# Kernel tuning notes

Measured on AMD Instinct MI355X. Metric: run time of the kernel, lower is better.

The kernel has to match this reference:

```python
import jax, jax.numpy as jnp
import numpy as np

H = 256
LATENT = 128
NODE_FEATS = (12, 5, 4)
EDGE_FEATS = (5, 4)
END_NODE = NODE_FEATS[0] - 1
MAX_NODES = 64


def setup_inputs() -> dict:
    key = jax.random.key(0)
    ks = iter(jax.random.split(key, 40))
    def rn(shape, s=0.1):
        return jax.random.normal(next(ks), shape, dtype=jnp.float32) * s
    inp = {
        "z": jax.random.normal(next(ks), (1, LATENT), dtype=jnp.float32),
        "lp_w": rn((H, LATENT)), "lp_b": rn((H,)),
        "nWih": rn((3 * H, H)), "nWhh": rn((3 * H, H)), "nbih": rn((3 * H,)), "nbhh": rn((3 * H,)),
        "eWih": rn((3 * H, H)), "eWhh": rn((3 * H, H)), "ebih": rn((3 * H,)), "ebhh": rn((3 * H,)),
    }
    for j, f in enumerate(NODE_FEATS):
        inp[f"nc{j}_w"] = rn((f, H)); inp[f"nc{j}_b"] = rn((f,))
    for j, f in enumerate(EDGE_FEATS):
        inp[f"ec{j}_w"] = rn((f, H)); inp[f"ec{j}_b"] = rn((f,))
    inp["max_nodes"] = MAX_NODES
    return inp


def _gru(x, h, Wih, Whh, bih, bhh):
    # torch.nn.GRU single step, single layer. x,h: (1,H)
    gi = x @ Wih.T + bih
    gh = h @ Whh.T + bhh
    ir, iz, inn = jnp.split(gi, 3, axis=-1)
    hr, hz, hn = jnp.split(gh, 3, axis=-1)
    r = jax.nn.sigmoid(ir + hr)
    zg = jax.nn.sigmoid(iz + hz)
    n = jnp.tanh(inn + r * hn)
    return (1.0 - zg) * n + zg * h


def _classify(emb, W, b):
    # Linear -> softmax -> (max prob, argmax), batch=1 -> scalars
    p = jax.nn.softmax(emb @ W.T + b, axis=-1)[0]
    return jnp.max(p), jnp.argmax(p)


def _generate(z, lp_w, lp_b, nWih, nWhh, nbih, nbhh, eWih, eWhh, ebih, ebhh,
              nc0_w, nc0_b, nc1_w, nc1_b, nc2_w, nc2_b,
              ec0_w, ec0_b, ec1_w, ec1_b, max_nodes):
    node_cls = ((nc0_w, nc0_b), (nc1_w, nc1_b), (nc2_w, nc2_b))
    edge_cls = ((ec0_w, ec0_b), (ec1_w, ec1_b))
    h0 = z @ lp_w.T + lp_b                     # latent_project; set_context
    buf0 = jnp.zeros((max_nodes, 1, H), z.dtype)  # node embedding history

    def step(carry, i):
        h, buf, done = carry
        x = jnp.where(i == 0, jnp.zeros((1, H), z.dtype), buf[jnp.maximum(i - 1, 0)])
        h1 = _gru(x, h, nWih, nWhh, nbih, nbhh)   # node_celli.forward_unit; emb = h1
        nps, nis = zip(*[_classify(h1, W, b) for W, b in node_cls])
        nprobs = jnp.stack(nps)                   # (3,)
        nidxs = jnp.stack(nis)                    # (3,) int
        is_end = nidxs[0] == END_NODE

        # edge cell: seq over previous node embeddings, most recent first
        def estep(he, t):
            valid = t < i
            src = jnp.clip(i - 1 - t, 0, max_nodes - 1)
            he2 = _gru(buf[src], he, eWih, eWhh, ebih, ebhh)
            he_new = jnp.where(valid, he2, he)
            eps, eis = zip(*[_classify(he_new, W, b) for W, b in edge_cls])
            return he_new, (jnp.stack(eps), jnp.stack(eis))

        he_fin, (ep_t, ei_t) = jax.lax.scan(estep, h1, jnp.arange(max_nodes))
        # reindex: edge for source node j was produced at inner step t = i-1-j
        js = jnp.arange(max_nodes)
        ts = jnp.clip(i - 1 - js, 0, max_nodes - 1)
        ep_row = ep_t[ts]                          # (max_nodes, 2)
        ei_row = ei_t[ts]
        vj = js < i
        no_edges = jnp.all(jnp.where(vj, ei_row[:, 0] == 0, True)) & (i > 0)

        active = jnp.logical_not(done)
        node_ok = active & jnp.logical_not(is_end) & jnp.logical_not(no_edges)
        done_new = done | is_end | no_edges

        h_next = jnp.where(node_ok & (i > 0), he_fin, h1)  # node hidden <- edge hidden
        h_next = jnp.where(active, h_next, h)
        buf_new = buf.at[i].set(jnp.where(node_ok, h1, buf[i]))

        edge_valid = vj & node_ok & (i > 0)
        out = (jnp.where(node_ok, nprobs, 0.0), nidxs, node_ok,
               jnp.where(edge_valid[:, None], ep_row, 0.0), ei_row, edge_valid)
        return (h_next, buf_new, done_new), out

    _, outs = jax.lax.scan(step, (h0, buf0, jnp.zeros((), bool)), jnp.arange(max_nodes))
    # node_probs (M,3), node_idxs (M,3), node_valid (M,),
    # edge_probs (M,M,2), edge_idxs (M,M,2), edge_valid (M,M)
    return outs


def reference(z, lp_w, lp_b, nWih, nWhh, nbih, nbhh, eWih, eWhh, ebih, ebhh,
              nc0_w, nc0_b, nc1_w, nc1_b, nc2_w, nc2_b,
              ec0_w, ec0_b, ec1_w, ec1_b, max_nodes):
    return _generate(z, lp_w, lp_b, nWih, nWhh, nbih, nbhh, eWih, eWhh, ebih, ebhh,
                     nc0_w, nc0_b, nc1_w, nc1_b, nc2_w, nc2_b,
                     ec0_w, ec0_b, ec1_w, ec1_b, max_nodes)
```

## Files before the change

kernel.cpp:

```cpp
#include <hip/hip_runtime.h>
#include <stdint.h>
#include <cstddef>


typedef unsigned int u32;

#define H 256
#define HL 128
#define G3 768
#define NW 16
#define SL 16
#define MAXN 64
#define NSTATE (1 + MAXN + (MAXN*(MAXN-1))/2)
#define SENTU 0xFFFFFFFFu
#define DEADV 0x0000DEADu

#define WG_CLS NW
#define WG_HELP0 (NW+1)
#define NHELP_PER 6
#define NROLE (WG_HELP0 + 2*NHELP_PER)
#define NWG 256

#define NP_OFF 0
#define NI_OFF 192
#define NV_OFF 384
#define EP_OFF 448
#define EI_OFF (EP_OFF + MAXN*MAXN*2)
#define EV_OFF (EI_OFF + MAXN*MAXN*2)

struct Wksp {
  float hP[NSTATE][H];
  float hS[NSTATE][H];
  float gi_e[MAXN][G3];
  float gi_n[MAXN][G3];
  u32 decP[MAXN];
  u32 decS[MAXN];
  u32 winner;
  u32 padw[7];
  u32 ticket[8];
};

union Shm {
  float force[26624];
  struct {
    float hcur[2][H];
    float bihe[3*SL], bhhe[3*SL], bihn[3*SL], bhhn[3*SL];
    float zv[HL];
    u32 dec;
  } w;
  struct {
    float cb[30];
    float hc[2][H];
    float logits[32];
    float np[3]; int ni[3];
    float ept[MAXN][2];
    int   eit[MAXN][2];
    u32 isend, bflag;
  } c;
  struct { float h1[H]; } hp;
};

__device__ __forceinline__ u32 ld_sc0(const u32* p) {
  u32 v;
  asm volatile("global_load_dword %0, %1, off sc0\n\ts_waitcnt vmcnt(0)"
               : "=&v"(v) : "v"(p) : "memory");
  return v;
}
__device__ __forceinline__ void st_sc0(u32* p, u32 v) {
  asm volatile("global_store_dword %0, %1, off sc0" :: "v"(p), "v"(v) : "memory");
}
__device__ __forceinline__ u32 ld_ag(const u32* p) {
  return __hip_atomic_load(p, __ATOMIC_RELAXED, __HIP_MEMORY_SCOPE_AGENT);
}
__device__ __forceinline__ void st_ag(u32* p, u32 v) {
  __hip_atomic_store(p, v, __ATOMIC_RELAXED, __HIP_MEMORY_SCOPE_AGENT);
}
__device__ __forceinline__ void pub2(u32* pp, u32* sp, u32 v, bool sc) {
  if (sc) st_sc0(pp, v);
  st_ag(sp, v);
}
__device__ __forceinline__ u32 spin2(const u32* pp, const u32* sp, bool sc) {
  if (sc) {
    #pragma unroll 1
    for (int i = 0; i < 16; ++i) {
      const u32 v = ld_sc0(pp);
      if (v != SENTU) return v;
    }
  }
  u32 v = ld_ag(sp);
  while (v == SENTU) v = ld_ag(sp);
  return v;
}
__device__ __forceinline__ float spin2f(const float* pp, const float* sp, bool sc) {
  return __uint_as_float(spin2((const u32*)pp, (const u32*)sp, sc));
}
__device__ __forceinline__ float spinf(const float* p) {
  u32 v = ld_ag((const u32*)p);
  while (v == SENTU) v = ld_ag((const u32*)p);
  return __uint_as_float(v);
}
__device__ __forceinline__ float spinf_slow(const float* p) {
  u32 v = ld_ag((const u32*)p);
  while (v == SENTU) {
    __builtin_amdgcn_s_sleep(1);
    v = ld_ag((const u32*)p);
  }
  return __uint_as_float(v);
}
__device__ __forceinline__ void pubf(float* p, float x) { st_ag((u32*)p, __float_as_uint(x)); }
__device__ __forceinline__ float sigm(float x) { return 1.0f / (1.0f + expf(-x)); }

__global__ __launch_bounds__(256, 1)
void Generator_34746285425383_kernel(
    const float* __restrict__ z, const float* __restrict__ lp_w, const float* __restrict__ lp_b,
    const float* __restrict__ nWih, const float* __restrict__ nWhh,
    const float* __restrict__ nbih, const float* __restrict__ nbhh,
    const float* __restrict__ eWih, const float* __restrict__ eWhh,
    const float* __restrict__ ebih, const float* __restrict__ ebhh,
    const float* __restrict__ nc0w, const float* __restrict__ nc0b,
    const float* __restrict__ nc1w, const float* __restrict__ nc1b,
    const float* __restrict__ nc2w, const float* __restrict__ nc2b,
    const float* __restrict__ ec0w, const float* __restrict__ ec0b,
    const float* __restrict__ ec1w, const float* __restrict__ ec1b,
    float* __restrict__ out, Wksp* __restrict__ ws)
{
  __shared__ Shm S;
  __shared__ int role_s, mode_s;
  const int tid = threadIdx.x;

  if (tid == 0) {
    u32 xcc;
    asm volatile("s_getreg_b32 %0, hwreg(HW_REG_XCC_ID)" : "=s"(xcc));
    xcc &= 7u;
    const u32 slot = __hip_atomic_fetch_add(&ws->ticket[xcc], 1u,
                        __ATOMIC_RELAXED, __HIP_MEMORY_SCOPE_AGENT);
    if (slot == NROLE - 1) {
      u32 exp = SENTU;
      __hip_atomic_compare_exchange_strong(&ws->winner, &exp, xcc,
          __ATOMIC_RELAXED, __ATOMIC_RELAXED, __HIP_MEMORY_SCOPE_AGENT);
    }
    u32 wv = ld_ag(&ws->winner);
    int iters = 0;
    while (wv == SENTU) {
      ++iters;
      if (iters > 1500 && blockIdx.x == 0) {
        u32 exp = SENTU;
        __hip_atomic_compare_exchange_strong(&ws->winner, &exp, DEADV,
            __ATOMIC_RELAXED, __ATOMIC_RELAXED, __HIP_MEMORY_SCOPE_AGENT);
      }
      wv = ld_ag(&ws->winner);
    }
    if (wv <= 7u) { role_s = (wv == xcc && slot < NROLE) ? (int)slot : -1; mode_s = 1; }
    else          { role_s = ((int)blockIdx.x < NROLE) ? (int)blockIdx.x : -1; mode_s = 0; }
  }
  __syncthreads();
  const int bid = role_s;
  const bool sc = (mode_s != 0);
  if (bid < 0) return;

  if (bid < NW) {
    const int w = bid, g = tid >> 4, c = tid & 15;
    const int k = w * SL + g;
    const bool gl = (c < 2);
    float wn0[16], wn1[16], wn2[16], we0[16], we1[16], we2[16];
    #pragma unroll
    for (int it = 0; it < 16; ++it) {
      const int col = c + 16 * it;
      wn0[it] = nWhh[(0 * H + k) * H + col];
      wn1[it] = nWhh[(1 * H + k) * H + col];
      wn2[it] = nWhh[(2 * H + k) * H + col];
      we0[it] = eWhh[(0 * H + k) * H + col];
      we1[it] = eWhh[(1 * H + k) * H + col];
      we2[it] = eWhh[(2 * H + k) * H + col];
    }
    if (tid < 3 * SL) {
      const int gate = tid / SL, gg = tid % SL;
      const int grow = gate * H + w * SL + gg;
      S.w.bihe[tid] = ebih[grow]; S.w.bhhe[tid] = ebhh[grow];
      S.w.bihn[tid] = nbih[grow]; S.w.bhhn[tid] = nbhh[grow];
    }
    if (tid < HL) S.w.zv[tid] = z[tid];
    __syncthreads();

    {
      float p = 0.f;
      for (int it = 0; it < 8; ++it) {
        const int col = c + 16 * it;
        p += S.w.zv[col] * lp_w[k * HL + col];
      }
      for (int off = 1; off < 16; off <<= 1) p += __shfl_xor(p, off);
      const float h0 = p + lp_b[k];
      if (c == 0 && sc) st_sc0((u32*)&ws->hP[0][k], __float_as_uint(h0));
      if (c == 1)       st_ag((u32*)&ws->hS[0][k], __float_as_uint(h0));
    }

    int m = 1, idx_carry = 0;
    bool done = false;
    unsigned long long valid = 0ull;
    float pg0 = 0.f, pg1 = 0.f, pg2 = 0.f;
    const float* pga = nullptr;

    for (int i = 0; i < MAXN; ++i) {
      for (int t = -1; t < i; ++t) {
        const bool is_node = (t < 0);
        const int hidx = is_node ? idx_carry : (m - 1);
        const int src  = is_node ? (i - 1) : (i - 1 - t);
        float* hc = S.w.hcur[m & 1];
        hc[tid] = spin2f(&ws->hP[hidx][tid], &ws->hS[hidx][tid], sc);
        float gi0 = 0.f, gi1 = 0.f, gi2 = 0.f;
        const bool use_gi = (src >= 0) && ((valid >> src) & 1ull);
        if (gl && use_gi) {
          gi0 = pg0; gi1 = pg1; gi2 = pg2;
          if (__float_as_uint(gi0) == SENTU) gi0 = spinf(&pga[0 * H + k]);
          if (__float_as_uint(gi1) == SENTU) gi1 = spinf(&pga[1 * H + k]);
          if (__float_as_uint(gi2) == SENTU) gi2 = spinf(&pga[2 * H + k]);
        }
        __syncthreads();
        float p0 = 0.f, p1 = 0.f, p2 = 0.f;
        if (is_node) {
          #pragma unroll
          for (int it = 0; it < 16; ++it) {
            const float hv = hc[c + 16 * it];
            p0 += wn0[it] * hv; p1 += wn1[it] * hv; p2 += wn2[it] * hv;
          }
        } else {
          #pragma unroll
          for (int it = 0; it < 16; ++it) {
            const float hv = hc[c + 16 * it];
            p0 += we0[it] * hv; p1 += we1[it] * hv; p2 += we2[it] * hv;
          }
        }
        for (int off = 1; off < 16; off <<= 1) {
          p0 += __shfl_xor(p0, off);
          p1 += __shfl_xor(p1, off);
          p2 += __shfl_xor(p2, off);
        }
        const float* bih = is_node ? S.w.bihn : S.w.bihe;
        const float* bhh = is_node ? S.w.bhhn : S.w.bhhe;
        const float rr = sigm(gi0 + bih[0 * SL + g] + p0 + bhh[0 * SL + g]);
        const float zz = sigm(gi1 + bih[1 * SL + g] + p1 + bhh[1 * SL + g]);
        const float nn = tanhf(gi2 + bih[2 * SL + g] + rr * (p2 + bhh[2 * SL + g]));
        const float hp = (1.f - zz) * nn + zz * hc[k];
        if (c == 0 && sc) st_sc0((u32*)&ws->hP[m][k], __float_as_uint(hp));
        if (c == 1)       st_ag((u32*)&ws->hS[m][k], __float_as_uint(hp));
        if (gl) {
          int ni = i, nt = t + 1;
          if (nt >= i) { ni = i + 1; nt = -1; }
          if (ni < MAXN) {
            const bool nnode = (nt < 0);
            const int nsrc = nnode ? (ni - 1) : (ni - 1 - nt);
            if (nsrc >= 0) {
              pga = nnode ? ws->gi_n[nsrc] : ws->gi_e[nsrc];
              pg0 = __builtin_nontemporal_load(&pga[0 * H + k]);
              pg1 = __builtin_nontemporal_load(&pga[1 * H + k]);
              pg2 = __builtin_nontemporal_load(&pga[2 * H + k]);
            }
          }
        }
        ++m;
      }
      if (tid == 0) S.w.dec = spin2(&ws->decP[i], &ws->decS[i], sc);
      __syncthreads();
      const u32 dec = S.w.dec;
      const bool is_end   = (dec >> 1) & 1u;
      const bool no_edges = (dec >> 2) & 1u;
      const bool active   = !done;
      const bool node_ok  = active && !is_end && !no_edges;
      if (node_ok) valid |= (1ull << i);
      const int s_end = m - 1, node_m = m - 1 - i;
      if (active) idx_carry = (node_ok && i > 0) ? s_end : node_m;
      done = done || is_end || no_edges;
    }

  } else if (bid == WG_CLS) {
    const int g = tid >> 4, c = tid & 15;
    const float* wsrc[5] = { nc0w, nc1w, nc2w, ec0w, ec1w };
    const float* bsrc[5] = { nc0b, nc1b, nc2b, ec0b, ec1b };
    const int hbase[5] = { 0, 12, 17, 21, 26 };
    float cw0[16], cw1[16];
    {
      const int r0 = g;
      const int h0i = r0 < 12 ? 0 : r0 < 17 ? 1 : r0 < 21 ? 2 : r0 < 26 ? 3 : 4;
      const float* W0 = wsrc[h0i];
      const int rr0 = r0 - hbase[h0i];
      const int r1 = g + 16;
      const int h1i = r1 < 17 ? 1 : r1 < 21 ? 2 : r1 < 26 ? 3 : 4;
      const float* W1 = wsrc[h1i];
      const int rr1 = r1 - hbase[h1i];
      const bool live1 = (r1 < 30);
      #pragma unroll
      for (int it = 0; it < 16; ++it) {
        const int col = c + 16 * it;
        cw0[it] = W0[rr0 * H + col];
        cw1[it] = live1 ? W1[rr1 * H + col] : 0.f;
      }
    }
    if (tid < 30) {
      const int hh = tid < 12 ? 0 : tid < 17 ? 1 : tid < 21 ? 2 : tid < 26 ? 3 : 4;
      S.c.cb[tid] = bsrc[hh][tid - hbase[hh]];
    }
    __syncthreads();

    int m = 1;
    bool done = false;
    for (int i = 0; i < MAXN; ++i) {
      for (int t = -1; t < i; ++t) {
        float* hcb = S.c.hc[m & 1];
        hcb[tid] = spin2f(&ws->hP[m][tid], &ws->hS[m][tid], sc);
        __syncthreads();
        {
          float p0 = 0.f, p1 = 0.f;
          #pragma unroll
          for (int it = 0; it < 16; ++it) {
            const float hv = hcb[c + 16 * it];
            p0 += cw0[it] * hv;
            p1 += cw1[it] * hv;
          }
          for (int off = 1; off < 16; off <<= 1) {
            p0 += __shfl_xor(p0, off);
            p1 += __shfl_xor(p1, off);
          }
          if (c == 0) {
            S.c.logits[g] = p0 + S.c.cb[g];
            if (g + 16 < 30) S.c.logits[g + 16] = p1 + S.c.cb[g + 16];
          }
        }
        __syncthreads();
        if (tid < 64) {
          const int lane = tid;
          int hh, j;
          if (lane < 16)      { hh = 0; j = lane;      }
          else if (lane < 24) { hh = 1; j = lane - 16; }
          else if (lane < 32) { hh = 2; j = lane - 24; }
          else if (lane < 40) { hh = 3; j = lane - 32; }
          else if (lane < 48) { hh = 4; j = lane - 40; }
          else                { hh = 4; j = 99; }
          const int hb = hbase[hh];
          const int hl = hh == 0 ? 12 : hh == 1 ? 5 : hh == 2 ? 4 : hh == 3 ? 5 : 4;
          const bool live = (j < hl);
          const float myl = live ? S.c.logits[hb + j] : -3.4e38f;
          float mx = myl; int idx = live ? j : 1000;
          #pragma unroll
          for (int mk = 1; mk <= 4; mk <<= 1) {
            const float lv = __shfl_xor(mx, mk);
            const int   iv = __shfl_xor(idx, mk);
            if (lv > mx || (lv == mx && iv < idx)) { mx = lv; idx = iv; }
          }
          { const float lv = __shfl_xor(mx, 8);
            const int   iv = __shfl_xor(idx, 8);
            if (lane < 16 && (lv > mx || (lv == mx && iv < idx))) { mx = lv; idx = iv; } }
          float e = live ? expf(myl - mx) : 0.f;
          #pragma unroll
          for (int mk = 1; mk <= 4; mk <<= 1) e += __shfl_xor(e, mk);
          { const float ev = __shfl_xor(e, 8); if (lane < 16) e += ev; }
          const float pm = 1.0f / e;
          if (t < 0) {
            if (lane == 0)  { S.c.np[0] = pm; S.c.ni[0] = idx;
                              S.c.isend = (idx == 11) ? 1u : 0u; }
            if (lane == 16) { S.c.np[1] = pm; S.c.ni[1] = idx; }
            if (lane == 24) { S.c.np[2] = pm; S.c.ni[2] = idx; }
            if (i == 0) {
              if (lane == 32) { S.c.ept[0][0] = pm; S.c.eit[0][0] = idx; }
              if (lane == 40) { S.c.ept[0][1] = pm; S.c.eit[0][1] = idx; }
            }
          } else {
            if (lane == 32) { S.c.ept[t][0] = pm; S.c.eit[t][0] = idx; }
            if (lane == 40) { S.c.ept[t][1] = pm; S.c.eit[t][1] = idx; }
          }
        }
        ++m;
      }
      __syncthreads();
      if (tid < 64) {
        const bool myok = (tid < i) ? (S.c.eit[tid][0] == 0) : true;
        const unsigned long long b = __ballot(myok);
        if (tid == 0) S.c.bflag = ((b == ~0ull) && (i > 0)) ? 1u : 0u;
      }
      __syncthreads();
      const bool is_end   = (S.c.isend != 0u);
      const bool no_edges = (S.c.bflag != 0u);
      const bool active   = !done;
      const bool node_ok  = active && !is_end && !no_edges;
      if (tid == 0) {
        const u32 d = 1u | (is_end ? 2u : 0u) | (no_edges ? 4u : 0u);
        pub2(&ws->decP[i], &ws->decS[i], d, sc);
      }
      if (tid < MAXN) {
        const int j = tid;
        const bool vj = j < i;
        const bool ev = vj && node_ok && (i > 0);
        const int tt = vj ? (i - 1 - j) : 0;
        out[EP_OFF + (i * MAXN + j) * 2 + 0] = ev ? S.c.ept[tt][0] : 0.f;
        out[EP_OFF + (i * MAXN + j) * 2 + 1] = ev ? S.c.ept[tt][1] : 0.f;
        out[EI_OFF + (i * MAXN + j) * 2 + 0] = (float)S.c.eit[tt][0];
        out[EI_OFF + (i * MAXN + j) * 2 + 1] = (float)S.c.eit[tt][1];
        out[EV_OFF + i * MAXN + j] = ev ? 1.f : 0.f;
      } else if (tid < MAXN + 8) {
        const int q = tid - MAXN;
        if (q < 3)       out[NP_OFF + i * 3 + q]       = node_ok ? S.c.np[q] : 0.f;
        else if (q < 6)  out[NI_OFF + i * 3 + (q - 3)] = (float)S.c.ni[q - 3];
        else if (q == 6) out[NV_OFF + i]               = node_ok ? 1.f : 0.f;
      }
      done = done || is_end || no_edges;
      __syncthreads();
    }

  } else {
    const int e = bid - WG_HELP0;
    const bool is_edge = (e < NHELP_PER);
    const int rowbase = (e % NHELP_PER) * 128;
    const float* Wih = is_edge ? eWih : nWih;
    float* gdst = is_edge ? &ws->gi_e[0][0] : &ws->gi_n[0][0];
    const int g = tid >> 4, c = tid & 15;
    int m_node = 1;
    for (int i = 0; i < MAXN; ++i) {
      S.hp.h1[tid] = spinf_slow(&ws->hS[m_node][tid]);
      __syncthreads();
      for (int rr = 0; rr < 8; ++rr) {
        const int row = rowbase + g * 8 + rr;
        float p = 0.f;
        #pragma unroll
        for (int u = 0; u < 4; ++u) {
          const float4 wv = *(const float4*)&Wih[row * H + c * 16 + u * 4];
          p += wv.x * S.hp.h1[c * 16 + u * 4 + 0]
             + wv.y * S.hp.h1[c * 16 + u * 4 + 1]
             + wv.z * S.hp.h1[c * 16 + u * 4 + 2]
             + wv.w * S.hp.h1[c * 16 + u * 4 + 3];
        }
        for (int off = 1; off < 16; off <<= 1) p += __shfl_xor(p, off);
        if (c == 0) pubf(&gdst[i * G3 + row], p);
      }
      __syncthreads();
      m_node += 1 + i;
    }
  }
}

extern "C" void kernel_launch(void* const* d_in, const int* in_sizes, int n_in,
                              void* d_out, int out_size, void* d_ws, size_t ws_size,
                              hipStream_t stream) {
  hipMemsetAsync(d_ws, 0xFF, offsetof(Wksp, ticket), stream);
  hipMemsetAsync((char*)d_ws + offsetof(Wksp, ticket), 0,
                 sizeof(Wksp) - offsetof(Wksp, ticket), stream);
  Generator_34746285425383_kernel<<<dim3(NWG), dim3(256), 0, stream>>>(
      (const float*)d_in[0],  (const float*)d_in[1],  (const float*)d_in[2],
      (const float*)d_in[3],  (const float*)d_in[4],  (const float*)d_in[5],
      (const float*)d_in[6],  (const float*)d_in[7],  (const float*)d_in[8],
      (const float*)d_in[9],  (const float*)d_in[10],
      (const float*)d_in[11], (const float*)d_in[12],
      (const float*)d_in[13], (const float*)d_in[14],
      (const float*)d_in[15], (const float*)d_in[16],
      (const float*)d_in[17], (const float*)d_in[18],
      (const float*)d_in[19], (const float*)d_in[20],
      (float*)d_out, (Wksp*)d_ws);
}
```

Before: 4.594 ms.

## Vectorize hidden-state polling with dwordx4 loads and shrink helper workgroups

The per-step poll of the published hidden state now uses 64 threads issuing 128-bit sc0 loads instead of 256 scalar spins, which should cut memory traffic and polling latency on the serial critical path. The prefetch of the next gi values is moved ahead of the barrier. The input-projection helpers drop from 12 to 4 workgroups, each computing 24 rows instead of 8. That frees CUs and reduces contention from helper spinning, but each helper now has more work per node step and could fall behind the main chain.

```diff
diff --git a/kernel.cpp b/kernel.cpp
--- a/kernel.cpp
+++ b/kernel.cpp
@@ -4,6 +4,7 @@
 
 
 typedef unsigned int u32;
+typedef u32 u32x4 __attribute__((ext_vector_type(4)));
 
 #define H 256
 #define HL 128
@@ -17,8 +18,8 @@
 
 #define WG_CLS NW
 #define WG_HELP0 (NW+1)
-#define NHELP_PER 6
-#define NROLE (WG_HELP0 + 2*NHELP_PER)
+#define NHELP 4
+#define NROLE (WG_HELP0 + NHELP)
 #define NWG 256
 
 #define NP_OFF 0
@@ -91,9 +92,6 @@
   while (v == SENTU) v = ld_ag(sp);
   return v;
 }
-__device__ __forceinline__ float spin2f(const float* pp, const float* sp, bool sc) {
-  return __uint_as_float(spin2((const u32*)pp, (const u32*)sp, sc));
-}
 __device__ __forceinline__ float spinf(const float* p) {
   u32 v = ld_ag((const u32*)p);
   while (v == SENTU) v = ld_ag((const u32*)p);
@@ -109,6 +107,31 @@
 }
 __device__ __forceinline__ void pubf(float* p, float x) { st_ag((u32*)p, __float_as_uint(x)); }
 __device__ __forceinline__ float sigm(float x) { return 1.0f / (1.0f + expf(-x)); }
+
+__device__ __forceinline__ float4 gather4(const float* rowP, const float* rowS,
+                                          int q4, bool sc) {
+  if (sc) {
+    const u32* p = (const u32*)(rowP + q4);
+    #pragma unroll 1
+    for (int it = 0; it < 32; ++it) {
+      u32x4 v;
+      asm volatile("global_load_dwordx4 %0, %1, off sc0\n\ts_waitcnt vmcnt(0)"
+                   : "=&v"(v) : "v"(p) : "memory");
+      if (v.x != SENTU && v.y != SENTU && v.z != SENTU && v.w != SENTU) {
+        float4 f;
+        f.x = __uint_as_float(v.x); f.y = __uint_as_float(v.y);
+        f.z = __uint_as_float(v.z); f.w = __uint_as_float(v.w);
+        return f;
+      }
+    }
+  }
+  float4 f;
+  f.x = spinf(rowS + q4 + 0);
+  f.y = spinf(rowS + q4 + 1);
+  f.z = spinf(rowS + q4 + 2);
+  f.w = spinf(rowS + q4 + 3);
+  return f;
+}
 
 __global__ __launch_bounds__(256, 1)
 void Generator_34746285425383_kernel(
@@ -206,7 +229,11 @@
         const int hidx = is_node ? idx_carry : (m - 1);
         const int src  = is_node ? (i - 1) : (i - 1 - t);
         float* hc = S.w.hcur[m & 1];
-        hc[tid] = spin2f(&ws->hP[hidx][tid], &ws->hS[hidx][tid], sc);
+        if (tid < 64) {
+          const int q4 = tid * 4;
+          const float4 f = gather4(ws->hP[hidx], ws->hS[hidx], q4, sc);
+          *(float4*)&hc[q4] = f;
+        }
         float gi0 = 0.f, gi1 = 0.f, gi2 = 0.f;
         const bool use_gi = (src >= 0) && ((valid >> src) & 1ull);
         if (gl && use_gi) {
@@ -215,34 +242,6 @@
           if (__float_as_uint(gi1) == SENTU) gi1 = spinf(&pga[1 * H + k]);
           if (__float_as_uint(gi2) == SENTU) gi2 = spinf(&pga[2 * H + k]);
         }
-        __syncthreads();
-        float p0 = 0.f, p1 = 0.f, p2 = 0.f;
-        if (is_node) {
-          #pragma unroll
-          for (int it = 0; it < 16; ++it) {
-            const float hv = hc[c + 16 * it];
-            p0 += wn0[it] * hv; p1 += wn1[it] * hv; p2 += wn2[it] * hv;
-          }
-        } else {
-          #pragma unroll
-          for (int it = 0; it < 16; ++it) {
-            const float hv = hc[c + 16 * it];
-            p0 += we0[it] * hv; p1 += we1[it] * hv; p2 += we2[it] * hv;
-          }
-        }
-        for (int off = 1; off < 16; off <<= 1) {
-          p0 += __shfl_xor(p0, off);
-          p1 += __shfl_xor(p1, off);
-          p2 += __shfl_xor(p2, off);
-        }
-        const float* bih = is_node ? S.w.bihn : S.w.bihe;
-        const float* bhh = is_node ? S.w.bhhn : S.w.bhhe;
-        const float rr = sigm(gi0 + bih[0 * SL + g] + p0 + bhh[0 * SL + g]);
-        const float zz = sigm(gi1 + bih[1 * SL + g] + p1 + bhh[1 * SL + g]);
-        const float nn = tanhf(gi2 + bih[2 * SL + g] + rr * (p2 + bhh[2 * SL + g]));
-        const float hp = (1.f - zz) * nn + zz * hc[k];
-        if (c == 0 && sc) st_sc0((u32*)&ws->hP[m][k], __float_as_uint(hp));
-        if (c == 1)       st_ag((u32*)&ws->hS[m][k], __float_as_uint(hp));
         if (gl) {
           int ni = i, nt = t + 1;
           if (nt >= i) { ni = i + 1; nt = -1; }
@@ -257,6 +256,34 @@
             }
           }
         }
+        __syncthreads();
+        float p0 = 0.f, p1 = 0.f, p2 = 0.f;
+        if (is_node) {
+          #pragma unroll
+          for (int it = 0; it < 16; ++it) {
+            const float hv = hc[c + 16 * it];
+            p0 += wn0[it] * hv; p1 += wn1[it] * hv; p2 += wn2[it] * hv;
+          }
+        } else {
+          #pragma unroll
+          for (int it = 0; it < 16; ++it) {
+            const float hv = hc[c + 16 * it];
+            p0 += we0[it] * hv; p1 += we1[it] * hv; p2 += we2[it] * hv;
+          }
+        }
+        for (int off = 1; off < 16; off <<= 1) {
+          p0 += __shfl_xor(p0, off);
+          p1 += __shfl_xor(p1, off);
+          p2 += __shfl_xor(p2, off);
+        }
+        const float* bih = is_node ? S.w.bihn : S.w.bihe;
+        const float* bhh = is_node ? S.w.bhhn : S.w.bhhe;
+        const float rr = sigm(gi0 + bih[0 * SL + g] + p0 + bhh[0 * SL + g]);
+        const float zz = sigm(gi1 + bih[1 * SL + g] + p1 + bhh[1 * SL + g]);
+        const float nn = tanhf(gi2 + bih[2 * SL + g] + rr * (p2 + bhh[2 * SL + g]));
+        const float hp = (1.f - zz) * nn + zz * hc[k];
+        if (c == 0 && sc) st_sc0((u32*)&ws->hP[m][k], __float_as_uint(hp));
+        if (c == 1)       st_ag((u32*)&ws->hS[m][k], __float_as_uint(hp));
         ++m;
       }
       if (tid == 0) S.w.dec = spin2(&ws->decP[i], &ws->decS[i], sc);
@@ -306,7 +333,11 @@
     for (int i = 0; i < MAXN; ++i) {
       for (int t = -1; t < i; ++t) {
         float* hcb = S.c.hc[m & 1];
-        hcb[tid] = spin2f(&ws->hP[m][tid], &ws->hS[m][tid], sc);
+        if (tid < 64) {
+          const int q4 = tid * 4;
+          const float4 f = gather4(ws->hP[m], ws->hS[m], q4, sc);
+          *(float4*)&hcb[q4] = f;
+        }
         __syncthreads();
         {
           float p0 = 0.f, p1 = 0.f;
@@ -407,8 +438,8 @@
 
   } else {
     const int e = bid - WG_HELP0;
-    const bool is_edge = (e < NHELP_PER);
-    const int rowbase = (e % NHELP_PER) * 128;
+    const bool is_edge = (e < 2);
+    const int rowbase = (e & 1) * 384;
     const float* Wih = is_edge ? eWih : nWih;
     float* gdst = is_edge ? &ws->gi_e[0][0] : &ws->gi_n[0][0];
     const int g = tid >> 4, c = tid & 15;
@@ -416,8 +447,8 @@
     for (int i = 0; i < MAXN; ++i) {
       S.hp.h1[tid] = spinf_slow(&ws->hS[m_node][tid]);
       __syncthreads();
-      for (int rr = 0; rr < 8; ++rr) {
-        const int row = rowbase + g * 8 + rr;
+      for (int rr = 0; rr < 24; ++rr) {
+        const int row = rowbase + g * 24 + rr;
         float p = 0.f;
         #pragma unroll
         for (int u = 0; u < 4; ++u) {
```

Measured after the change: 9.710 ms. 111% more time.
